# Kernel tuning notes

Hardware: AMD Instinct MI355X
Metric: run time of the kernel (lower is better)

The kernel has to match this reference:

```python
import jax, jax.numpy as jnp
import numpy as np
from functools import partial

B, T, D, H, V, L, NL = 2, 2048, 512, 8, 32000, 4, 3
HID = 4 * D
HD = D // H
EPS = 1e-5


def layernorm(x, g, b):
    mu = jnp.mean(x, axis=-1, keepdims=True)
    var = jnp.mean(jnp.square(x - mu), axis=-1, keepdims=True)
    return (x - mu) * jax.lax.rsqrt(var + EPS) * g + b


def self_mod_attn(x, Wq, Wk, Wv, Wo):
    # x: [B,T,D]; W*: [D,D] (applied as x @ W)
    def heads(w):
        return jnp.transpose((x @ w).reshape(B, T, H, HD), (1, 0, 2, 3))  # [T,B,H,HD]
    q, k, v = heads(Wq), heads(Wk), heads(Wv)

    def step(mem, qkv):
        q_t, k_t, v_t = qkv  # each [B,H,HD]
        mem = mem + jnp.einsum('bhd,bhk->hdk', v_t, k_t) / B  # batch-mean outer product
        y_t = jnp.einsum('hdk,bhk->bhd', mem, q_t)
        return mem, y_t

    mem0 = jnp.zeros((H, HD, HD), dtype=x.dtype)
    _, ys = jax.lax.scan(step, mem0, (q, k, v))  # ys: [T,B,H,HD]
    out = jnp.transpose(ys, (1, 0, 2, 3)).reshape(B, T, D)
    return out @ Wo


def cms(x, W1, b1, W2, b2):
    # Continuum memory system: NL parallel MLP levels (dim -> 4*dim -> dim, GELU), averaged.
    h = jax.nn.gelu(jnp.einsum('btd,ndh->nbth', x, W1) + b1[:, None, None, :])
    y = jnp.einsum('nbth,nhd->nbtd', h, W2) + b2[:, None, None, :]
    return jnp.mean(y, axis=0)


def setup_inputs() -> dict:
    key = jax.random.key(0)
    ks = jax.random.split(key, 16)
    std = 0.02
    p = {
        'emb': jax.random.normal(ks[0], (V, D), jnp.float32) * std,
        'pos': jax.random.normal(ks[1], (2048, D), jnp.float32) * std,
        'ln1_g': jnp.ones((L, D)), 'ln1_b': jnp.zeros((L, D)),
        'Wq': jax.random.normal(ks[2], (L, D, D), jnp.float32) * std,
        'Wk': jax.random.normal(ks[3], (L, D, D), jnp.float32) * std,
        'Wv': jax.random.normal(ks[4], (L, D, D), jnp.float32) * std,
        'Wo': jax.random.normal(ks[5], (L, D, D), jnp.float32) * std,
        'ln2_g': jnp.ones((L, D)), 'ln2_b': jnp.zeros((L, D)),
        'cms_W1': jax.random.normal(ks[6], (L, NL, D, HID), jnp.float32) * std,
        'cms_b1': jnp.zeros((L, NL, HID)),
        'cms_W2': jax.random.normal(ks[7], (L, NL, HID, D), jnp.float32) * std,
        'cms_b2': jnp.zeros((L, NL, D)),
        'lnf_g': jnp.ones((D,)), 'lnf_b': jnp.zeros((D,)),
        'input_ids': jax.random.randint(ks[8], (B, T), 0, V, jnp.int32),
    }
    return p


def reference(emb, pos, ln1_g, ln1_b, Wq, Wk, Wv, Wo, ln2_g, ln2_b,
              cms_W1, cms_b1, cms_W2, cms_b2, lnf_g, lnf_b, input_ids):
    x = emb[input_ids] + pos[:T][None, :, :]  # [B,T,D]
    for l in range(L):
        x = x + self_mod_attn(layernorm(x, ln1_g[l], ln1_b[l]), Wq[l], Wk[l], Wv[l], Wo[l])
        x = x + cms(layernorm(x, ln2_g[l], ln2_b[l]), cms_W1[l], cms_b1[l], cms_W2[l], cms_b2[l])
    x = layernorm(x, lnf_g, lnf_b)
    logits = x @ emb.T  # tied head, [B,T,V]
    return logits
```

## Files before the change

kernel.cpp:

```cpp
#include <hip/hip_runtime.h>
#include <stdint.h>

#define B_ 2
#define T_ 2048
#define D_ 512
#define H_ 8
#define HD_ 64
#define V_ 32000
#define L_ 4
#define NL_ 3
#define HID_ 2048
#define NROW 4096
#define CCH 64
#define CROWS 128
#define NC 32
#define EPS_ 1e-5f

typedef __attribute__((ext_vector_type(8))) __bf16 bf16x8;
typedef __attribute__((ext_vector_type(4))) float f32x4;

__device__ __forceinline__ float b2f(unsigned short u) {
  union { uint32_t i; float f; } v; v.i = ((uint32_t)u) << 16; return v.f;
}
__device__ __forceinline__ unsigned short f2b(float f) {
  union { float f; uint32_t i; } v; v.f = f;
  uint32_t u = v.i;
  u += 0x7fffu + ((u >> 16) & 1u);
  return (unsigned short)(u >> 16);
}

__global__ __launch_bounds__(256) void k_prep(
    const float* __restrict__ emb, const float* __restrict__ pos,
    const int* __restrict__ ids,
    const float* __restrict__ Wq, const float* __restrict__ Wk,
    const float* __restrict__ Wv, const float* __restrict__ Wo,
    const float* __restrict__ W1, const float* __restrict__ W2,
    const float* __restrict__ b2,
    const float* __restrict__ ln1g, const float* __restrict__ ln1b,
    unsigned short* __restrict__ WqkvT, unsigned short* __restrict__ WoT,
    unsigned short* __restrict__ W1T, unsigned short* __restrict__ W2cat,
    unsigned short* __restrict__ embB, float* __restrict__ bsum,
    float* __restrict__ x, unsigned short* __restrict__ h) {
  int bid = blockIdx.x, tid = threadIdx.x;
  __shared__ float tile[32][33];
  __shared__ float red[4], red2[4];
  int tx = tid & 31, ty = tid >> 5;
  if (bid < 4096) {
    int z = bid >> 8, r = bid & 255;
    int bx = (r & 15) * 32, by = (r >> 4) * 32;
    const float* in; unsigned short* out;
    if (z < 12) {
      int l = z / 3, m = z - l * 3;
      in = (m == 0 ? Wq : m == 1 ? Wk : Wv) + (size_t)l * D_ * D_;
      out = WqkvT + (size_t)z * D_ * D_;
    } else {
      in = Wo + (size_t)(z - 12) * D_ * D_;
      out = WoT + (size_t)(z - 12) * D_ * D_;
    }
#pragma unroll
    for (int i = 0; i < 4; i++)
      tile[ty + 8 * i][tx] = in[(size_t)(by + ty + 8 * i) * D_ + bx + tx];
    __syncthreads();
#pragma unroll
    for (int i = 0; i < 4; i++)
      out[(size_t)(bx + ty + 8 * i) * D_ + by + tx] = f2b(tile[tx][ty + 8 * i]);
  } else if (bid < 16384) {
    int s = bid - 4096;
    int z = s >> 10, r = s & 1023;
    int bx = (r & 63) * 32, by = (r >> 6) * 32;
    const float* in = W1 + (size_t)z * D_ * HID_;
    unsigned short* out = W1T + (size_t)z * HID_ * D_;
#pragma unroll
    for (int i = 0; i < 4; i++)
      tile[ty + 8 * i][tx] = in[(size_t)(by + ty + 8 * i) * HID_ + bx + tx];
    __syncthreads();
#pragma unroll
    for (int i = 0; i < 4; i++)
      out[(size_t)(bx + ty + 8 * i) * D_ + by + tx] = f2b(tile[tx][ty + 8 * i]);
  } else if (bid < 28672) {
    int s = bid - 16384;
    int z = s >> 10, r = s & 1023;
    int l = z / 3, n = z - l * 3;
    int bx = (r & 15) * 32, by = (r >> 4) * 32;
    const float* in = W2 + (size_t)z * HID_ * D_;
#pragma unroll
    for (int i = 0; i < 4; i++)
      tile[ty + 8 * i][tx] = in[(size_t)(by + ty + 8 * i) * D_ + bx + tx];
    __syncthreads();
#pragma unroll
    for (int i = 0; i < 4; i++)
      W2cat[((size_t)l * D_ + bx + ty + 8 * i) * (NL_ * HID_) + n * HID_ + by + tx] =
          f2b(tile[tx][ty + 8 * i]);
  } else if (bid < 44672) {
    int s = bid - 28672;
    int base = (s * 256 + tid) * 4;
    float4 v = *(const float4*)(emb + base);
    unsigned short o[4] = { f2b(v.x), f2b(v.y), f2b(v.z), f2b(v.w) };
    *(uint2*)(embB + base) = *(const uint2*)o;
  } else if (bid < 46720) {
    int s = bid - 44672;
    int i = s * 256 + tid;
    int row = i >> 7, cg = i & 127;
    int t = row & (T_ - 1);
    int id = ids[row];
    float4 e = ((const float4*)(emb + (size_t)id * D_))[cg];
    float4 p = ((const float4*)(pos + (size_t)t * D_))[cg];
    float4 xv; xv.x = e.x + p.x; xv.y = e.y + p.y; xv.z = e.z + p.z; xv.w = e.w + p.w;
    ((float4*)(x + (size_t)row * D_))[cg] = xv;
    float sum = xv.x + xv.y + xv.z + xv.w;
#pragma unroll
    for (int o = 32; o >= 1; o >>= 1) sum += __shfl_xor(sum, o);
    int wv = tid >> 6;
    if ((tid & 63) == 0) red[wv] = sum;
    __syncthreads();
    int wb = (tid >> 7) * 2;
    float mu = (red[wb] + red[wb + 1]) * (1.f / D_);
    float dx = xv.x - mu, dy = xv.y - mu, dz = xv.z - mu, dw = xv.w - mu;
    float s2 = dx * dx + dy * dy + dz * dz + dw * dw;
#pragma unroll
    for (int o = 32; o >= 1; o >>= 1) s2 += __shfl_xor(s2, o);
    if ((tid & 63) == 0) red2[wv] = s2;
    __syncthreads();
    float var = (red2[wb] + red2[wb + 1]) * (1.f / D_);
    float rs = rsqrtf(var + EPS_);
    float4 gv = ((const float4*)ln1g)[cg];
    float4 bv = ((const float4*)ln1b)[cg];
    unsigned short o4[4] = { f2b(dx * rs * gv.x + bv.x), f2b(dy * rs * gv.y + bv.y),
                             f2b(dz * rs * gv.z + bv.z), f2b(dw * rs * gv.w + bv.w) };
    *(uint2*)(h + (size_t)row * D_ + cg * 4) = *(const uint2*)o4;
  } else {
    int s = bid - 46720;
    int l = s >> 1, d = (s & 1) * 256 + tid;
    float acc = 0.f;
#pragma unroll
    for (int n = 0; n < NL_; n++) acc += b2[((size_t)l * NL_ + n) * D_ + d];
    bsum[(size_t)l * D_ + d] = acc;
  }
}

__global__ __launch_bounds__(128) void k_ln(
    const float* __restrict__ x, const float* __restrict__ g,
    const float* __restrict__ b, unsigned short* __restrict__ out) {
  int row = blockIdx.x;
  int tid = threadIdx.x;
  const float* xr = x + (size_t)row * D_;
  float4 v = ((const float4*)xr)[tid];
  float s = v.x + v.y + v.z + v.w;
#pragma unroll
  for (int o = 32; o >= 1; o >>= 1) s += __shfl_xor(s, o);
  __shared__ float red[2], red2[2];
  int wv = tid >> 6;
  if ((tid & 63) == 0) red[wv] = s;
  __syncthreads();
  float mu = (red[0] + red[1]) * (1.f / D_);
  float dx = v.x - mu, dy = v.y - mu, dz = v.z - mu, dw = v.w - mu;
  float s2 = dx * dx + dy * dy + dz * dz + dw * dw;
#pragma unroll
  for (int o = 32; o >= 1; o >>= 1) s2 += __shfl_xor(s2, o);
  if ((tid & 63) == 0) red2[wv] = s2;
  __syncthreads();
  float var = (red2[0] + red2[1]) * (1.f / D_);
  float rs = rsqrtf(var + EPS_);
  float4 gv = ((const float4*)g)[tid];
  float4 bv = ((const float4*)b)[tid];
  unsigned short o4[4] = { f2b(dx * rs * gv.x + bv.x), f2b(dy * rs * gv.y + bv.y),
                           f2b(dz * rs * gv.z + bv.z), f2b(dw * rs * gv.w + bv.w) };
  *(uint2*)(out + (size_t)row * D_ + tid * 4) = *(const uint2*)o4;
}

__global__ __launch_bounds__(256) void k_cmsred_ln(
    float* __restrict__ x, const float* __restrict__ parts,
    const float* __restrict__ bsum, const float* __restrict__ g,
    const float* __restrict__ b, unsigned short* __restrict__ h) {
  int bid = blockIdx.x, tid = threadIdx.x;
  int row = bid * 2 + (tid >> 7);
  int cg = tid & 127;
  size_t base = (size_t)row * D_ + cg * 4;
  float4 xv = *(const float4*)(x + base);
  float4 p0 = *(const float4*)(parts + base);
  float4 p1 = *(const float4*)(parts + (size_t)NROW * D_ + base);
  float4 p2 = *(const float4*)(parts + 2ull * NROW * D_ + base);
  float4 bs = *(const float4*)(bsum + cg * 4);
  const float k3 = 1.f / 3.f;
  xv.x += (p0.x + p1.x + p2.x + bs.x) * k3;
  xv.y += (p0.y + p1.y + p2.y + bs.y) * k3;
  xv.z += (p0.z + p1.z + p2.z + bs.z) * k3;
  xv.w += (p0.w + p1.w + p2.w + bs.w) * k3;
  *(float4*)(x + base) = xv;
  float sum = xv.x + xv.y + xv.z + xv.w;
#pragma unroll
  for (int o = 32; o >= 1; o >>= 1) sum += __shfl_xor(sum, o);
  __shared__ float red[4], red2[4];
  int wv = tid >> 6;
  if ((tid & 63) == 0) red[wv] = sum;
  __syncthreads();
  int wb = (tid >> 7) * 2;
  float mu = (red[wb] + red[wb + 1]) * (1.f / D_);
  float dx = xv.x - mu, dy = xv.y - mu, dz = xv.z - mu, dw = xv.w - mu;
  float s2 = dx * dx + dy * dy + dz * dz + dw * dw;
#pragma unroll
  for (int o = 32; o >= 1; o >>= 1) s2 += __shfl_xor(s2, o);
  if ((tid & 63) == 0) red2[wv] = s2;
  __syncthreads();
  float var = (red2[wb] + red2[wb + 1]) * (1.f / D_);
  float rs = rsqrtf(var + EPS_);
  float4 gv = ((const float4*)g)[cg];
  float4 bv = ((const float4*)b)[cg];
  unsigned short o4[4] = { f2b(dx * rs * gv.x + bv.x), f2b(dy * rs * gv.y + bv.y),
                           f2b(dz * rs * gv.z + bv.z), f2b(dw * rs * gv.w + bv.w) };
  *(uint2*)(h + base) = *(const uint2*)o4;
}

enum { E_QKV = 0, E_RES = 1, E_GELU = 2, E_PART = 3, E_F32 = 4 };

template <int TR, int NW>
__device__ __forceinline__ void stage_tile(
    const unsigned short* __restrict__ gbase, int ldk, unsigned short* lds,
    int wave, int lane) {
#pragma unroll
  for (int q = 0; q < 4; q++) {
    int Lb = (q * NW + wave) << 10;
    int L = Lb + lane * 16;
    int row = L >> 7;
    int colb = (L & 127) ^ ((row & 7) << 4);
    const unsigned short* gsrc = gbase + (size_t)row * ldk + (colb >> 1);
    __builtin_amdgcn_global_load_lds(
        (const __attribute__((address_space(1))) uint32_t*)gsrc,
        (__attribute__((address_space(3))) uint32_t*)(lds + (Lb >> 1)),
        16, 0, 0);
  }
}

template <int EPI>
__global__ __launch_bounds__(256, 2) void k_gemm128(
    const unsigned short* __restrict__ A,
    const unsigned short* __restrict__ Bt,
    const float* __restrict__ bias,
    void* __restrict__ Out,
    int Kext, int ldk, int N, int ldOut) {
  int z = blockIdx.z;
  A  += (size_t)z * Kext;
  Bt += (size_t)z * Kext;
  int lane = threadIdx.x & 63, wave = threadIdx.x >> 6;
  int wm = wave >> 1, wn = wave & 1;
  int bx = blockIdx.x, by = blockIdx.y;

  __shared__ __align__(16) unsigned short As[2][128 * 64];
  __shared__ __align__(16) unsigned short Bs[2][128 * 64];

  const unsigned short* Ab = A + (size_t)by * 128 * ldk;
  const unsigned short* Bb = Bt + (size_t)bx * 128 * ldk;

  f32x4 acc[4][4] = {};
  int nk = Kext / 64;
  stage_tile<128, 4>(Ab, ldk, As[0], wave, lane);
  stage_tile<128, 4>(Bb, ldk, Bs[0], wave, lane);
  __syncthreads();
  for (int kt = 0; kt < nk; kt++) {
    int cur = kt & 1;
    if (kt + 1 < nk) {
      stage_tile<128, 4>(Ab + (size_t)(kt + 1) * 64, ldk, As[cur ^ 1], wave, lane);
      stage_tile<128, 4>(Bb + (size_t)(kt + 1) * 64, ldk, Bs[cur ^ 1], wave, lane);
    }
    const char* Ac = (const char*)As[cur];
    const char* Bc = (const char*)Bs[cur];
#pragma unroll
    for (int kk = 0; kk < 2; kk++) {
      bf16x8 af[4], bfr[4];
#pragma unroll
      for (int mt = 0; mt < 4; mt++) {
        int row = wm * 64 + mt * 16 + (lane & 15);
        int off = ((row << 7) | (kk * 64 + ((lane >> 4) << 4))) ^ ((row & 7) << 4);
        af[mt] = *(const bf16x8*)(Ac + off);
      }
#pragma unroll
      for (int nt = 0; nt < 4; nt++) {
        int row = wn * 64 + nt * 16 + (lane & 15);
        int off = ((row << 7) | (kk * 64 + ((lane >> 4) << 4))) ^ ((row & 7) << 4);
        bfr[nt] = *(const bf16x8*)(Bc + off);
      }
#pragma unroll
      for (int mt = 0; mt < 4; mt++)
#pragma unroll
        for (int nt = 0; nt < 4; nt++)
          acc[mt][nt] = __builtin_amdgcn_mfma_f32_16x16x32_bf16(
              af[mt], bfr[nt], acc[mt][nt], 0, 0, 0);
    }
    __syncthreads();
  }

  int gm = by * 128 + wm * 64;
  int gn = bx * 128 + wn * 64;
#pragma unroll
  for (int mt = 0; mt < 4; mt++) {
#pragma unroll
    for (int nt = 0; nt < 4; nt++) {
      int m0 = gm + mt * 16 + ((lane >> 4) << 2);
      int n = gn + nt * 16 + (lane & 15);
#pragma unroll
      for (int j = 0; j < 4; j++) {
        float v = acc[mt][nt][j];
        int m = m0 + j;
        if constexpr (EPI == E_QKV) {
          int zq = n >> 9, col = n & 511;
          ((unsigned short*)Out)[((size_t)zq * NROW + m) * D_ + col] = f2b(v);
        } else if constexpr (EPI == E_RES) {
          size_t idx = (size_t)m * ldOut + n;
          ((float*)Out)[idx] = bias[idx] + v;
        } else if constexpr (EPI == E_GELU) {
          size_t idx = (size_t)m * ldOut + n;
          v += bias[n];
          float u2 = 1.5957691216057308f * (v + 0.044715f * v * v * v);
          float sg = 1.f / (1.f + __expf(-u2));
          ((unsigned short*)Out)[idx] = f2b(v * sg);
        } else {
          ((float*)Out)[(size_t)z * NROW * D_ + (size_t)m * ldOut + n] = v;
        }
      }
    }
  }
}

__global__ __launch_bounds__(512) void k_gemm256(
    const unsigned short* __restrict__ A,
    const unsigned short* __restrict__ Bt,
    void* __restrict__ Out,
    int K, int N, int ldOut) {
  int lane = threadIdx.x & 63, wave = threadIdx.x >> 6;
  int wm = wave >> 2, wn = wave & 3;
  int lin = blockIdx.y * 125 + blockIdx.x;
  int seg = lin / 400, rem = lin % 400;
  int bx = seg * 25 + rem % 25, by = rem / 25;

  __shared__ __align__(16) unsigned short As[256 * 64];
  __shared__ __align__(16) unsigned short Bs[256 * 64];

  const unsigned short* Ab = A + (size_t)by * 256 * K;
  const unsigned short* Bb = Bt + (size_t)bx * 256 * K;

  f32x4 acc[8][4] = {};
  int nk = K / 64;
  for (int kt = 0; kt < nk; kt++) {
    stage_tile<256, 8>(Ab + (size_t)kt * 64, K, As, wave, lane);
    stage_tile<256, 8>(Bb + (size_t)kt * 64, K, Bs, wave, lane);
    __syncthreads();
    const char* Ac = (const char*)As;
    const char* Bc = (const char*)Bs;
#pragma unroll
    for (int kk = 0; kk < 2; kk++) {
      bf16x8 af[8], bfr[4];
#pragma unroll
      for (int mt = 0; mt < 8; mt++) {
        int row = wm * 128 + mt * 16 + (lane & 15);
        int off = ((row << 7) | (kk * 64 + ((lane >> 4) << 4))) ^ ((row & 7) << 4);
        af[mt] = *(const bf16x8*)(Ac + off);
      }
#pragma unroll
      for (int nt = 0; nt < 4; nt++) {
        int row = wn * 64 + nt * 16 + (lane & 15);
        int off = ((row << 7) | (kk * 64 + ((lane >> 4) << 4))) ^ ((row & 7) << 4);
        bfr[nt] = *(const bf16x8*)(Bc + off);
      }
#pragma unroll
      for (int mt = 0; mt < 8; mt++)
#pragma unroll
        for (int nt = 0; nt < 4; nt++)
          acc[mt][nt] = __builtin_amdgcn_mfma_f32_16x16x32_bf16(
              af[mt], bfr[nt], acc[mt][nt], 0, 0, 0);
    }
    __syncthreads();
  }

  int gm = by * 256 + wm * 128;
  int gn = bx * 256 + wn * 64;
#pragma unroll
  for (int mt = 0; mt < 8; mt++) {
#pragma unroll
    for (int nt = 0; nt < 4; nt++) {
      int m0 = gm + mt * 16 + ((lane >> 4) << 2);
      int n = gn + nt * 16 + (lane & 15);
#pragma unroll
      for (int j = 0; j < 4; j++)
        ((float*)Out)[(size_t)(m0 + j) * ldOut + n] = acc[mt][nt][j];
    }
  }
}

__device__ __forceinline__ void unpack8f(uint4 u, float* dst) {
  dst[0] = b2f((unsigned short)(u.x & 0xffff)); dst[1] = b2f((unsigned short)(u.x >> 16));
  dst[2] = b2f((unsigned short)(u.y & 0xffff)); dst[3] = b2f((unsigned short)(u.y >> 16));
  dst[4] = b2f((unsigned short)(u.z & 0xffff)); dst[5] = b2f((unsigned short)(u.z >> 16));
  dst[6] = b2f((unsigned short)(u.w & 0xffff)); dst[7] = b2f((unsigned short)(u.w >> 16));
}

__global__ __launch_bounds__(256) void k_attnA(
    const unsigned short* __restrict__ kbuf, const unsigned short* __restrict__ vbuf,
    float* __restrict__ G) {
  int c = blockIdx.x, h = blockIdx.y;
  __shared__ __align__(16) float Ks[CROWS][HD_];
  __shared__ __align__(16) float Vs[CROWS][HD_];
  int tid = threadIdx.x;
#pragma unroll
  for (int it = 0; it < 4; it++) {
    int gi = it * 256 + tid;
    int r = gi >> 3, c8 = gi & 7;
    int bb = r & 1, tt = c * CCH + (r >> 1);
    size_t goff = ((size_t)bb * T_ + tt) * D_ + h * HD_ + c8 * 8;
    uint4 kv = *(const uint4*)(kbuf + goff);
    uint4 vv = *(const uint4*)(vbuf + goff);
    unpack8f(kv, &Ks[r][c8 * 8]);
    unpack8f(vv, &Vs[r][c8 * 8]);
  }
  __syncthreads();
  int d = tid & 63, kb = (tid >> 6) * 16;
  float acc[16] = {};
  for (int r = 0; r < CROWS; r++) {
    float vd = Vs[r][d];
#pragma unroll
    for (int j = 0; j < 16; j++) acc[j] += vd * Ks[r][kb + j];
  }
  float* Gp = G + (((size_t)c * H_ + h) * HD_ + d) * HD_ + kb;
#pragma unroll
  for (int j = 0; j < 16; j++) Gp[j] = 0.5f * acc[j];
}

__global__ __launch_bounds__(256) void k_attnB(const float* __restrict__ G,
                                               float* __restrict__ Mem) {
  int hh = blockIdx.x >> 4, seg = blockIdx.x & 15;
  int idx = seg * 256 + threadIdx.x;
  float g[NC];
#pragma unroll
  for (int c = 0; c < NC; c++)
    g[c] = G[((size_t)c * H_ + hh) * (HD_ * HD_) + idx];
  float m = 0.f;
#pragma unroll
  for (int c = 0; c < NC; c++) {
    Mem[((size_t)c * H_ + hh) * (HD_ * HD_) + idx] = m;
    m += g[c];
  }
}

__global__ __launch_bounds__(256) void k_attnC(
    const unsigned short* __restrict__ qbuf, const unsigned short* __restrict__ kbuf,
    const unsigned short* __restrict__ vbuf, const float* __restrict__ Mem,
    unsigned short* __restrict__ ybuf) {
  int c = blockIdx.x, h = blockIdx.y;
  __shared__ __align__(16) unsigned short smem[32768];
  unsigned short* Qs  = smem;
  unsigned short* Ksh = smem + 8192;
  unsigned short* Vt  = smem + 16384;
  unsigned short* Mhi = smem + 24576;
  unsigned short* Mlo = smem + 28672;
  unsigned short* Ps  = smem;

  int tid = threadIdx.x, lane = tid & 63, w = tid >> 6;
#pragma unroll
  for (int it = 0; it < 4; it++) {
    int gi = it * 256 + tid;
    int r = gi >> 3, g8 = gi & 7;
    int bb = r & 1, tt = c * CCH + (r >> 1);
    size_t go = ((size_t)bb * T_ + tt) * D_ + h * HD_ + g8 * 8;
    int qc = (g8 * 8) ^ ((r & 7) << 3);
    *(uint4*)(Qs + r * 64 + qc) = *(const uint4*)(qbuf + go);
    *(uint4*)(Ksh + r * 64 + qc) = *(const uint4*)(kbuf + go);
    uint4 vv = *(const uint4*)(vbuf + go);
    const unsigned short* vp = (const unsigned short*)&vv;
#pragma unroll
    for (int j = 0; j < 8; j++) {
      int d = g8 * 8 + j;
      int t = (d & 7) ^ (d >> 3);
      Vt[d * 128 + (r ^ (t << 3))] = vp[j];
    }
  }
  {
    const float* Mp = Mem + (((size_t)c * H_ + h) << 12);
#pragma unroll
    for (int it = 0; it < 16; it++) {
      int i = it * 256 + tid;
      int d = i >> 6, k = i & 63;
      float m = Mp[i];
      unsigned short hi = f2b(m);
      float lo = m - b2f(hi);
      int col = k ^ ((d & 7) << 3);
      Mhi[d * 64 + col] = hi;
      Mlo[d * 64 + col] = f2b(lo);
    }
  }
  __syncthreads();

  int row0 = w * 32;
  f32x4 sacc[2][8] = {};
  f32x4 yacc[2][4] = {};
#pragma unroll
  for (int kk = 0; kk < 2; kk++) {
    bf16x8 aq[2];
#pragma unroll
    for (int mt = 0; mt < 2; mt++) {
      int row = row0 + mt * 16 + (lane & 15);
      aq[mt] = *(const bf16x8*)(Qs + row * 64 +
                ((kk * 32 + ((lane >> 4) << 3)) ^ ((row & 7) << 3)));
    }
#pragma unroll
    for (int nt = 0; nt < 8; nt++) {
      int row = nt * 16 + (lane & 15);
      bf16x8 bk = *(const bf16x8*)(Ksh + row * 64 +
                ((kk * 32 + ((lane >> 4) << 3)) ^ ((row & 7) << 3)));
#pragma unroll
      for (int mt = 0; mt < 2; mt++)
        sacc[mt][nt] = __builtin_amdgcn_mfma_f32_16x16x32_bf16(aq[mt], bk,
                                                               sacc[mt][nt], 0, 0, 0);
    }
#pragma unroll
    for (int nt = 0; nt < 4; nt++) {
      int row = nt * 16 + (lane & 15);
      int off = row * 64 + ((kk * 32 + ((lane >> 4) << 3)) ^ ((row & 7) << 3));
      bf16x8 bh = *(const bf16x8*)(Mhi + off);
      bf16x8 bl = *(const bf16x8*)(Mlo + off);
#pragma unroll
      for (int mt = 0; mt < 2; mt++) {
        yacc[mt][nt] = __builtin_amdgcn_mfma_f32_16x16x32_bf16(aq[mt], bh,
                                                               yacc[mt][nt], 0, 0, 0);
        yacc[mt][nt] = __builtin_amdgcn_mfma_f32_16x16x32_bf16(aq[mt], bl,
                                                               yacc[mt][nt], 0, 0, 0);
      }
    }
  }
  __syncthreads();

#pragma unroll
  for (int mt = 0; mt < 2; mt++)
#pragma unroll
    for (int nt = 0; nt < 8; nt++)
#pragma unroll
      for (int j = 0; j < 4; j++) {
        int qr = row0 + mt * 16 + ((lane >> 4) << 2) + j;
        int ks = nt * 16 + (lane & 15);
        float v = ((ks >> 1) <= (qr >> 1)) ? sacc[mt][nt][j] * 0.5f : 0.f;
        Ps[qr * 128 + (ks ^ ((qr & 7) << 3))] = f2b(v);
      }
  __syncthreads();

  for (int kb = 0; kb <= w; kb++) {
    bf16x8 ap[2];
#pragma unroll
    for (int mt = 0; mt < 2; mt++) {
      int row = row0 + mt * 16 + (lane & 15);
      ap[mt] = *(const bf16x8*)(Ps + row * 128 +
                ((kb * 32 + ((lane >> 4) << 3)) ^ ((row & 7) << 3)));
    }
#pragma unroll
    for (int nt = 0; nt < 4; nt++) {
      int d = nt * 16 + (lane & 15);
      int t = (d & 7) ^ (d >> 3);
      int gb = (kb * 32 + ((lane >> 4) << 3)) ^ (t << 3);
      bf16x8 bv = *(const bf16x8*)(Vt + d * 128 + gb);
#pragma unroll
      for (int mt = 0; mt < 2; mt++)
        yacc[mt][nt] = __builtin_amdgcn_mfma_f32_16x16x32_bf16(ap[mt], bv,
                                                               yacc[mt][nt], 0, 0, 0);
    }
  }

#pragma unroll
  for (int mt = 0; mt < 2; mt++)
#pragma unroll
    for (int nt = 0; nt < 4; nt++)
#pragma unroll
      for (int j = 0; j < 4; j++) {
        int qr = row0 + mt * 16 + ((lane >> 4) << 2) + j;
        int d = nt * 16 + (lane & 15);
        int bb = qr & 1, tl = qr >> 1;
        ybuf[((size_t)bb * T_ + c * CCH + tl) * D_ + h * HD_ + d] =
            f2b(yacc[mt][nt][j]);
      }
}

extern "C" void kernel_launch(void* const* d_in, const int* in_sizes, int n_in,
                              void* d_out, int out_size, void* d_ws, size_t ws_size,
                              hipStream_t stream) {
  (void)in_sizes; (void)n_in; (void)out_size; (void)ws_size;
  const float* emb  = (const float*)d_in[0];
  const float* pos  = (const float*)d_in[1];
  const float* ln1g = (const float*)d_in[2];
  const float* ln1b = (const float*)d_in[3];
  const float* Wq   = (const float*)d_in[4];
  const float* Wk   = (const float*)d_in[5];
  const float* Wv   = (const float*)d_in[6];
  const float* Wo   = (const float*)d_in[7];
  const float* ln2g = (const float*)d_in[8];
  const float* ln2b = (const float*)d_in[9];
  const float* W1   = (const float*)d_in[10];
  const float* b1   = (const float*)d_in[11];
  const float* W2   = (const float*)d_in[12];
  const float* b2   = (const float*)d_in[13];
  const float* lnfg = (const float*)d_in[14];
  const float* lnfb = (const float*)d_in[15];
  const int*   ids  = (const int*)d_in[16];

  char* w = (char*)d_ws;
  size_t off = 0;
  auto alloc = [&](size_t bytes) -> void* {
    void* p = w + off; off += (bytes + 255) & ~(size_t)255; return p;
  };
  const size_t DD = (size_t)D_ * D_;
  unsigned short* WqkvT = (unsigned short*)alloc(12ull * DD * 2);
  unsigned short* WoT   = (unsigned short*)alloc(4ull * DD * 2);
  unsigned short* W1T   = (unsigned short*)alloc((size_t)L_ * NL_ * HID_ * D_ * 2);
  unsigned short* W2cat = (unsigned short*)alloc((size_t)L_ * D_ * NL_ * HID_ * 2);
  unsigned short* embB  = (unsigned short*)alloc((size_t)V_ * D_ * 2);
  float* bsum           = (float*)alloc((size_t)L_ * D_ * 4);
  float* x              = (float*)alloc((size_t)NROW * D_ * 4);
  unsigned short* h     = (unsigned short*)alloc((size_t)NROW * D_ * 2);
  unsigned short* qkv   = (unsigned short*)alloc(3ull * NROW * D_ * 2);
  unsigned short* ybuf  = (unsigned short*)alloc((size_t)NROW * D_ * 2);
  float* G              = (float*)alloc((size_t)NC * H_ * HD_ * HD_ * 4);
  float* Mem            = (float*)alloc((size_t)NC * H_ * HD_ * HD_ * 4);
  float* parts          = (float*)qkv;
  unsigned short* hmid  = (unsigned short*)alloc((size_t)NROW * NL_ * HID_ * 2);

  dim3 blk(256);
  k_prep<<<dim3(46728), blk, 0, stream>>>(emb, pos, ids, Wq, Wk, Wv, Wo, W1, W2, b2,
                                          ln1g, ln1b,
                                          WqkvT, WoT, W1T, W2cat, embB, bsum, x, h);

  unsigned short* qb = qkv;
  unsigned short* kb = qkv + (size_t)NROW * D_;
  unsigned short* vb = qkv + 2ull * NROW * D_;

  for (int l = 0; l < L_; l++) {
    k_gemm128<E_QKV><<<dim3(12, 32), blk, 0, stream>>>(
        h, WqkvT + (size_t)l * 3 * DD, bsum, qkv, D_, D_, 3 * D_, D_);
    k_attnA<<<dim3(NC, H_), blk, 0, stream>>>(kb, vb, G);
    k_attnB<<<dim3(H_ * 16), blk, 0, stream>>>(G, Mem);
    k_attnC<<<dim3(NC, H_), blk, 0, stream>>>(qb, kb, vb, Mem, ybuf);
    k_gemm128<E_RES><<<dim3(4, 32), blk, 0, stream>>>(
        ybuf, WoT + (size_t)l * DD, x, x, D_, D_, D_, D_);
    k_ln<<<dim3(NROW), dim3(128), 0, stream>>>(x, ln2g + l * D_, ln2b + l * D_, h);
    k_gemm128<E_GELU><<<dim3(48, 32), blk, 0, stream>>>(
        h, W1T + (size_t)l * NL_ * HID_ * D_, b1 + (size_t)l * NL_ * HID_, hmid,
        D_, D_, NL_ * HID_, NL_ * HID_);
    k_gemm128<E_PART><<<dim3(4, 32, 3), blk, 0, stream>>>(
        hmid, W2cat + (size_t)l * D_ * NL_ * HID_, bsum, parts,
        2048, NL_ * HID_, D_, D_);
    const float* gn = (l < 3) ? (ln1g + (l + 1) * D_) : lnfg;
    const float* bn = (l < 3) ? (ln1b + (l + 1) * D_) : lnfb;
    k_cmsred_ln<<<dim3(NROW / 2), blk, 0, stream>>>(x, parts, bsum + l * D_, gn, bn, h);
  }
  k_gemm256<<<dim3(125, 16), dim3(512), 0, stream>>>(h, embB, d_out, D_, V_, V_);
}
```

Measured before the change: 919.2 us.

## Use 256-tile GEMM for CMS up-projection, add XCD block remap, vectorize attnA

```diff
diff --git a/kernel.cpp b/kernel.cpp
--- a/kernel.cpp
+++ b/kernel.cpp
@@ -231,6 +231,15 @@
   }
 }
 
+__device__ __forceinline__ void xcd_remap(int& bx, int& by) {
+  int gx = gridDim.x;
+  int nwg = gx * gridDim.y;
+  int lin = by * gx + bx;
+  int q = nwg >> 3;
+  int nl = (lin & 7) * q + (lin >> 3);
+  bx = nl % gx;  by = nl / gx;
+}
+
 template <int EPI>
 __global__ __launch_bounds__(256, 2) void k_gemm128(
     const unsigned short* __restrict__ A,
@@ -244,6 +253,7 @@
   int lane = threadIdx.x & 63, wave = threadIdx.x >> 6;
   int wm = wave >> 1, wn = wave & 1;
   int bx = blockIdx.x, by = blockIdx.y;
+  xcd_remap(bx, by);
 
   __shared__ __align__(16) unsigned short As[2][128 * 64];
   __shared__ __align__(16) unsigned short Bs[2][128 * 64];
@@ -307,81 +317,92 @@
         } else if constexpr (EPI == E_RES) {
           size_t idx = (size_t)m * ldOut + n;
           ((float*)Out)[idx] = bias[idx] + v;
-        } else if constexpr (EPI == E_GELU) {
-          size_t idx = (size_t)m * ldOut + n;
+        } else {
+          ((float*)Out)[(size_t)z * NROW * D_ + (size_t)m * ldOut + n] = v;
+        }
+      }
+    }
+  }
+}
+
+template <int EPI>
+__global__ __launch_bounds__(512) void k_gemm256(
+    const unsigned short* __restrict__ A,
+    const unsigned short* __restrict__ Bt,
+    const float* __restrict__ bias,
+    void* __restrict__ Out,
+    int K, int N, int ldOut) {
+  int lane = threadIdx.x & 63, wave = threadIdx.x >> 6;
+  int wm = wave >> 2, wn = wave & 3;
+  int bx = blockIdx.x, by = blockIdx.y;
+  if constexpr (EPI == E_F32) {
+    int lin = blockIdx.y * 125 + blockIdx.x;
+    int seg = lin / 400, rem = lin % 400;
+    bx = seg * 25 + rem % 25;  by = rem / 25;
+  } else {
+    xcd_remap(bx, by);
+  }
+
+  __shared__ __align__(16) unsigned short As[256 * 64];
+  __shared__ __align__(16) unsigned short Bs[256 * 64];
+
+  const unsigned short* Ab = A + (size_t)by * 256 * K;
+  const unsigned short* Bb = Bt + (size_t)bx * 256 * K;
+
+  f32x4 acc[8][4] = {};
+  int nk = K / 64;
+  for (int kt = 0; kt < nk; kt++) {
+    stage_tile<256, 8>(Ab + (size_t)kt * 64, K, As, wave, lane);
+    stage_tile<256, 8>(Bb + (size_t)kt * 64, K, Bs, wave, lane);
+    __syncthreads();
+    const char* Ac = (const char*)As;
+    const char* Bc = (const char*)Bs;
+#pragma unroll
+    for (int kk = 0; kk < 2; kk++) {
+      bf16x8 af[8], bfr[4];
+#pragma unroll
+      for (int mt = 0; mt < 8; mt++) {
+        int row = wm * 128 + mt * 16 + (lane & 15);
+        int off = ((row << 7) | (kk * 64 + ((lane >> 4) << 4))) ^ ((row & 7) << 4);
+        af[mt] = *(const bf16x8*)(Ac + off);
+      }
+#pragma unroll
+      for (int nt = 0; nt < 4; nt++) {
+        int row = wn * 64 + nt * 16 + (lane & 15);
+        int off = ((row << 7) | (kk * 64 + ((lane >> 4) << 4))) ^ ((row & 7) << 4);
+        bfr[nt] = *(const bf16x8*)(Bc + off);
+      }
+#pragma unroll
+      for (int mt = 0; mt < 8; mt++)
+#pragma unroll
+        for (int nt = 0; nt < 4; nt++)
+          acc[mt][nt] = __builtin_amdgcn_mfma_f32_16x16x32_bf16(
+              af[mt], bfr[nt], acc[mt][nt], 0, 0, 0);
+    }
+    __syncthreads();
+  }
+
+  int gm = by * 256 + wm * 128;
+  int gn = bx * 256 + wn * 64;
+#pragma unroll
+  for (int mt = 0; mt < 8; mt++) {
+#pragma unroll
+    for (int nt = 0; nt < 4; nt++) {
+      int m0 = gm + mt * 16 + ((lane >> 4) << 2);
+      int n = gn + nt * 16 + (lane & 15);
+#pragma unroll
+      for (int j = 0; j < 4; j++) {
+        float v = acc[mt][nt][j];
+        size_t idx = (size_t)(m0 + j) * ldOut + n;
+        if constexpr (EPI == E_GELU) {
           v += bias[n];
           float u2 = 1.5957691216057308f * (v + 0.044715f * v * v * v);
           float sg = 1.f / (1.f + __expf(-u2));
           ((unsigned short*)Out)[idx] = f2b(v * sg);
         } else {
-          ((float*)Out)[(size_t)z * NROW * D_ + (size_t)m * ldOut + n] = v;
+          ((float*)Out)[idx] = v;
         }
       }
-    }
-  }
-}
-
-__global__ __launch_bounds__(512) void k_gemm256(
-    const unsigned short* __restrict__ A,
-    const unsigned short* __restrict__ Bt,
-    void* __restrict__ Out,
-    int K, int N, int ldOut) {
-  int lane = threadIdx.x & 63, wave = threadIdx.x >> 6;
-  int wm = wave >> 2, wn = wave & 3;
-  int lin = blockIdx.y * 125 + blockIdx.x;
-  int seg = lin / 400, rem = lin % 400;
-  int bx = seg * 25 + rem % 25, by = rem / 25;
-
-  __shared__ __align__(16) unsigned short As[256 * 64];
-  __shared__ __align__(16) unsigned short Bs[256 * 64];
-
-  const unsigned short* Ab = A + (size_t)by * 256 * K;
-  const unsigned short* Bb = Bt + (size_t)bx * 256 * K;
-
-  f32x4 acc[8][4] = {};
-  int nk = K / 64;
-  for (int kt = 0; kt < nk; kt++) {
-    stage_tile<256, 8>(Ab + (size_t)kt * 64, K, As, wave, lane);
-    stage_tile<256, 8>(Bb + (size_t)kt * 64, K, Bs, wave, lane);
-    __syncthreads();
-    const char* Ac = (const char*)As;
-    const char* Bc = (const char*)Bs;
-#pragma unroll
-    for (int kk = 0; kk < 2; kk++) {
-      bf16x8 af[8], bfr[4];
-#pragma unroll
-      for (int mt = 0; mt < 8; mt++) {
-        int row = wm * 128 + mt * 16 + (lane & 15);
-        int off = ((row << 7) | (kk * 64 + ((lane >> 4) << 4))) ^ ((row & 7) << 4);
-        af[mt] = *(const bf16x8*)(Ac + off);
-      }
-#pragma unroll
-      for (int nt = 0; nt < 4; nt++) {
-        int row = wn * 64 + nt * 16 + (lane & 15);
-        int off = ((row << 7) | (kk * 64 + ((lane >> 4) << 4))) ^ ((row & 7) << 4);
-        bfr[nt] = *(const bf16x8*)(Bc + off);
-      }
-#pragma unroll
-      for (int mt = 0; mt < 8; mt++)
-#pragma unroll
-        for (int nt = 0; nt < 4; nt++)
-          acc[mt][nt] = __builtin_amdgcn_mfma_f32_16x16x32_bf16(
-              af[mt], bfr[nt], acc[mt][nt], 0, 0, 0);
-    }
-    __syncthreads();
-  }
-
-  int gm = by * 256 + wm * 128;
-  int gn = bx * 256 + wn * 64;
-#pragma unroll
-  for (int mt = 0; mt < 8; mt++) {
-#pragma unroll
-    for (int nt = 0; nt < 4; nt++) {
-      int m0 = gm + mt * 16 + ((lane >> 4) << 2);
-      int n = gn + nt * 16 + (lane & 15);
-#pragma unroll
-      for (int j = 0; j < 4; j++)
-        ((float*)Out)[(size_t)(m0 + j) * ldOut + n] = acc[mt][nt][j];
     }
   }
 }
@@ -416,8 +437,12 @@
   float acc[16] = {};
   for (int r = 0; r < CROWS; r++) {
     float vd = Vs[r][d];
-#pragma unroll
-    for (int j = 0; j < 16; j++) acc[j] += vd * Ks[r][kb + j];
+    const float4* Kr = (const float4*)(&Ks[r][kb]);
+    float4 k0 = Kr[0], k1 = Kr[1], k2 = Kr[2], k3 = Kr[3];
+    acc[0] += vd * k0.x;  acc[1] += vd * k0.y;  acc[2] += vd * k0.z;  acc[3] += vd * k0.w;
+    acc[4] += vd * k1.x;  acc[5] += vd * k1.y;  acc[6] += vd * k1.z;  acc[7] += vd * k1.w;
+    acc[8] += vd * k2.x;  acc[9] += vd * k2.y;  acc[10] += vd * k2.z; acc[11] += vd * k2.w;
+    acc[12] += vd * k3.x; acc[13] += vd * k3.y; acc[14] += vd * k3.z; acc[15] += vd * k3.w;
   }
   float* Gp = G + (((size_t)c * H_ + h) * HD_ + d) * HD_ + kb;
 #pragma unroll
@@ -636,9 +661,9 @@
     k_gemm128<E_RES><<<dim3(4, 32), blk, 0, stream>>>(
         ybuf, WoT + (size_t)l * DD, x, x, D_, D_, D_, D_);
     k_ln<<<dim3(NROW), dim3(128), 0, stream>>>(x, ln2g + l * D_, ln2b + l * D_, h);
-    k_gemm128<E_GELU><<<dim3(48, 32), blk, 0, stream>>>(
+    k_gemm256<E_GELU><<<dim3(24, 16), dim3(512), 0, stream>>>(
         h, W1T + (size_t)l * NL_ * HID_ * D_, b1 + (size_t)l * NL_ * HID_, hmid,
-        D_, D_, NL_ * HID_, NL_ * HID_);
+        D_, NL_ * HID_, NL_ * HID_);
     k_gemm128<E_PART><<<dim3(4, 32, 3), blk, 0, stream>>>(
         hmid, W2cat + (size_t)l * D_ * NL_ * HID_, bsum, parts,
         2048, NL_ * HID_, D_, D_);
@@ -646,5 +671,6 @@
     const float* bn = (l < 3) ? (ln1b + (l + 1) * D_) : lnfb;
     k_cmsred_ln<<<dim3(NROW / 2), blk, 0, stream>>>(x, parts, bsum + l * D_, gn, bn, h);
   }
-  k_gemm256<<<dim3(125, 16), dim3(512), 0, stream>>>(h, embB, d_out, D_, V_, V_);
-}
+  k_gemm256<E_F32><<<dim3(125, 16), dim3(512), 0, stream>>>(
+      h, embB, bsum, d_out, D_, V_, V_);
+}
```

Result: slower. 971.3 us (+5.7%).
